# Optimization experiments

Measured on AMD Instinct MI355X. Metric: run time of the kernel, lower is better.

## Reference

```python
import jax, jax.numpy as jnp
import numpy as np

H = 8          # query heads
KVH = 1        # key/value heads
HD = 256       # head dim
ROPE_BASE = 10000.0


def _rotate_half(x):
    x1, x2 = x[..., : HD // 2], x[..., HD // 2 :]
    return jnp.concatenate((-x2, x1), axis=-1)


def _rope_cos_sin(position_ids):
    # position_ids: [B, S] int -> cos/sin: [B, S, HD]
    inv_freq = 1.0 / (ROPE_BASE ** (jnp.arange(0, HD, 2, dtype=jnp.float32) / HD))
    freqs = position_ids.astype(jnp.float32)[..., None] * inv_freq  # [B,S,HD/2]
    emb = jnp.concatenate((freqs, freqs), axis=-1)                  # [B,S,HD]
    return jnp.cos(emb), jnp.sin(emb)


def setup_inputs() -> dict:
    key = jax.random.key(0)
    ks = jax.random.split(key, 5)
    B, S, D = 2, 2048, 2048
    return {
        "hidden_states": jax.random.normal(ks[0], (B, S, D), dtype=jnp.float32),
        "attention_mask": jnp.zeros((B, 1, S, S), dtype=jnp.float32),
        "position_ids": jnp.broadcast_to(jnp.arange(S, dtype=jnp.int32), (B, S)),
        "Wq": jax.random.normal(ks[1], (D, H * HD), dtype=jnp.float32) * 0.02,
        "Wk": jax.random.normal(ks[2], (D, KVH * HD), dtype=jnp.float32) * 0.02,
        "Wv": jax.random.normal(ks[3], (D, KVH * HD), dtype=jnp.float32) * 0.02,
        "Wo": jax.random.normal(ks[4], (H * HD, D), dtype=jnp.float32) * 0.02,
    }


def reference(hidden_states, attention_mask, position_ids, Wq, Wk, Wv, Wo):
    B, S, D = hidden_states.shape
    # projections -> [B, heads, S, HD]
    q = jnp.einsum("bsd,df->bsf", hidden_states, Wq).reshape(B, S, H, HD).transpose(0, 2, 1, 3)
    k = jnp.einsum("bsd,df->bsf", hidden_states, Wk).reshape(B, S, KVH, HD).transpose(0, 2, 1, 3)
    v = jnp.einsum("bsd,df->bsf", hidden_states, Wv).reshape(B, S, KVH, HD).transpose(0, 2, 1, 3)

    cos, sin = _rope_cos_sin(position_ids)
    cos, sin = cos[:, None], sin[:, None]  # unsqueeze head dim
    q = q * cos + _rotate_half(q) * sin
    k = k * cos + _rotate_half(k) * sin

    # GQA: repeat kv heads to match query heads
    rep = H // KVH
    k = jnp.repeat(k, rep, axis=1)
    v = jnp.repeat(v, rep, axis=1)

    d_k = D // H  # matches torch code's scaling (== HD here)
    scores = jnp.einsum("bhqd,bhkd->bhqk", q, k) / jnp.sqrt(jnp.float32(d_k))
    scores = scores + attention_mask
    attn = jax.nn.softmax(scores, axis=-1)  # dropout p=0 / eval mode

    out = jnp.einsum("bhqk,bhkd->bhqd", attn, v)  # [B,H,S,HD]
    out = out.transpose(0, 2, 1, 3).reshape(B, S, H * HD)
    out = jnp.einsum("bsf,fd->bsd", out, Wo)
    return out
```

## Files before the change

kernel.cpp:

```cpp
#include <hip/hip_runtime.h>
#include <cmath>


typedef __bf16 bf16;
typedef __attribute__((ext_vector_type(8))) __bf16 bf16x8;
typedef __attribute__((ext_vector_type(4))) __bf16 bf16x4;
typedef __attribute__((ext_vector_type(4))) float f32x4;

#define S_LEN 2048
#define D_MODEL 2048
#define H_NUM 8
#define HDIM 256
#define KP 264
#define VP2 72

__device__ __forceinline__ void gl_lds16(const bf16* g, bf16* l) {
  __builtin_amdgcn_global_load_lds(
      (const __attribute__((address_space(1))) void*)g,
      (__attribute__((address_space(3))) void*)l, 16, 0, 0);
}

__global__ void cvt_bf16(const float* __restrict__ src, bf16* __restrict__ dst) {
  const int i = (blockIdx.x * 256 + threadIdx.x) * 4;
  const float4 v = *(const float4*)(src + i);
  bf16x4 o;
  o[0] = (bf16)v.x; o[1] = (bf16)v.y; o[2] = (bf16)v.z; o[3] = (bf16)v.w;
  *(bf16x4*)(dst + i) = o;
}

__global__ void tpose_cvt(const float* __restrict__ W, bf16* __restrict__ Wt,
                          int Ncols, int no0) {
  __shared__ float t[32][33];
  const int tx = threadIdx.x, ty = threadIdx.y;
  const int n0 = blockIdx.x * 32, k0 = blockIdx.y * 32;
#pragma unroll
  for (int i = 0; i < 4; ++i)
    t[ty + 8 * i][tx] = W[(size_t)(k0 + ty + 8 * i) * Ncols + (n0 + tx)];
  __syncthreads();
#pragma unroll
  for (int i = 0; i < 4; ++i)
    Wt[(size_t)(no0 + n0 + ty + 8 * i) * D_MODEL + (k0 + tx)] = (bf16)t[tx][ty + 8 * i];
}

__global__ __launch_bounds__(256)
void gemm_bf16(const bf16* __restrict__ A, const bf16* __restrict__ Wt,
               bf16* __restrict__ Cq, bf16* __restrict__ Ck, bf16* __restrict__ Cv,
               float* __restrict__ Cf, int M, int N, int mode) {
  __shared__ bf16 As[128 * 32];
  __shared__ bf16 Bs[128 * 32];
  const int tid = threadIdx.x;
  const int lane = tid & 63;
  const int wbase = tid & 192;
  const int c16 = lane & 15;
  const int quad = lane >> 4;
  const int wave = tid >> 6;
  const int wr = wave >> 1, wc = wave & 1;
  const int m0 = blockIdx.y * 128, n0 = blockIdx.x * 128;

  f32x4 acc[4][4];
#pragma unroll
  for (int i = 0; i < 4; ++i)
#pragma unroll
    for (int j = 0; j < 4; ++j)
#pragma unroll
      for (int r = 0; r < 4; ++r) acc[i][j][r] = 0.f;

  for (int k0 = 0; k0 < D_MODEL; k0 += 32) {
#pragma unroll
    for (int j = 0; j < 2; ++j) {
      const int bslot = j * 256 + wbase;
      const int slot = bslot + lane;
      const int row = slot >> 2, ch = slot & 3;
      gl_lds16(&A[(size_t)(m0 + row) * D_MODEL + k0 + ch * 8], &As[bslot * 8]);
      gl_lds16(&Wt[(size_t)(n0 + row) * D_MODEL + k0 + ch * 8], &Bs[bslot * 8]);
    }
    __syncthreads();
    bf16x8 af[4], bfr[4];
#pragma unroll
    for (int i = 0; i < 4; ++i)
      af[i] = *(const bf16x8*)&As[(wr * 64 + i * 16 + c16) * 32 + quad * 8];
#pragma unroll
    for (int j = 0; j < 4; ++j)
      bfr[j] = *(const bf16x8*)&Bs[(wc * 64 + j * 16 + c16) * 32 + quad * 8];
#pragma unroll
    for (int i = 0; i < 4; ++i)
#pragma unroll
      for (int j = 0; j < 4; ++j)
        acc[i][j] = __builtin_amdgcn_mfma_f32_16x16x32_bf16(af[i], bfr[j], acc[i][j], 0, 0, 0);
    __syncthreads();
  }

#pragma unroll
  for (int i = 0; i < 4; ++i)
#pragma unroll
    for (int j = 0; j < 4; ++j) {
      const int n = n0 + wc * 64 + j * 16 + c16;
#pragma unroll
      for (int r = 0; r < 4; ++r) {
        const int m = m0 + wr * 64 + i * 16 + quad * 4 + r;
        const float val = acc[i][j][r];
        if (mode == 1) {
          const int b = m >> 11, s = m & 2047;
          if (n0 < 2048) {
            const int h = n >> 8, hd = n & 255;
            Cq[((((size_t)b * H_NUM + h) * S_LEN + s) << 8) + hd] = (bf16)val;
          } else if (n0 < 2304) {
            Ck[((size_t)m << 8) + (n - 2048)] = (bf16)val;
          } else {
            Cv[((size_t)((b << 8) + (n - 2304)) << 11) + s] = (bf16)val;
          }
        } else {
          Cf[(size_t)m * D_MODEL + n] = val;
        }
      }
    }
}

#define ROPE_C (-0.07195578415606394f)

__global__ void rope_q_bf16(bf16* __restrict__ q, const int* __restrict__ pos) {
  const int idx = blockIdx.x * 256 + threadIdx.x;
  const int j = idx & 127;
  const int t = idx >> 7;
  const int s = t & 2047;
  const int bh = t >> 11;
  const int b = bh >> 3;
  const float p = (float)pos[(b << 11) + s];
  float sn, cs;
  sincosf(p * expf((float)j * ROPE_C), &sn, &cs);
  bf16* base = q + (((size_t)bh << 11) + s) * HDIM;
  const float x1 = (float)base[j], x2 = (float)base[j + 128];
  base[j] = (bf16)(x1 * cs - x2 * sn);
  base[j + 128] = (bf16)(x2 * cs + x1 * sn);
}

__global__ void rope_k_bf16(bf16* __restrict__ k, const int* __restrict__ pos) {
  const int idx = blockIdx.x * 256 + threadIdx.x;
  const int j = idx & 127;
  const int t = idx >> 7;
  const int s = t & 2047;
  const int b = t >> 11;
  const float p = (float)pos[(b << 11) + s];
  float sn, cs;
  sincosf(p * expf((float)j * ROPE_C), &sn, &cs);
  bf16* base = k + (size_t)t * HDIM;
  const float x1 = (float)base[j], x2 = (float)base[j + 128];
  base[j] = (bf16)(x1 * cs - x2 * sn);
  base[j + 128] = (bf16)(x2 * cs + x1 * sn);
}

__global__ __launch_bounds__(256, 2)
void flash_bf16(const bf16* __restrict__ qg, const bf16* __restrict__ kg,
                const bf16* __restrict__ vg, const float* __restrict__ msk,
                bf16* __restrict__ ao) {
  __shared__ bf16 Ks[64 * KP];
  __shared__ bf16 Vs[256 * VP2];
  __shared__ bf16 Ps[64 * VP2];

  const int tid = threadIdx.x;
  const int lane = tid & 63;
  const int w = tid >> 6;
  const int c16 = lane & 15;
  const int quad = lane >> 4;

  const int qbi = blockIdx.x & 31;
  const int h = (blockIdx.x >> 5) & 7;
  const int b = blockIdx.x >> 8;
  const int q0 = qbi * 64;

  const bf16* qbase = qg + ((((size_t)b * H_NUM + h) * S_LEN + q0) << 8);
  const bf16* kbase = kg + ((size_t)b << 19);
  const bf16* vbase = vg + ((size_t)b << 19);
  const float* mbase = msk + (size_t)b * S_LEN * S_LEN +
                       (size_t)(q0 + w * 16 + quad * 4) * S_LEN;

  bf16x8 qf[8];
#pragma unroll
  for (int kd = 0; kd < 8; ++kd)
    qf[kd] = *(const bf16x8*)&qbase[((w * 16 + c16) << 8) + kd * 32 + quad * 8];

  f32x4 oacc[16];
#pragma unroll
  for (int t = 0; t < 16; ++t)
#pragma unroll
    for (int r = 0; r < 4; ++r) oacc[t][r] = 0.f;
  float mrow[4] = {-1e30f, -1e30f, -1e30f, -1e30f};
  float lrow[4] = {0.f, 0.f, 0.f, 0.f};

  for (int k0 = 0; k0 < S_LEN; k0 += 64) {
    float ml[4][4];
#pragma unroll
    for (int ct = 0; ct < 4; ++ct)
#pragma unroll
      for (int r = 0; r < 4; ++r)
        ml[ct][r] = mbase[(size_t)r * S_LEN + k0 + ct * 16 + c16];

    __syncthreads();
#pragma unroll
    for (int i = 0; i < 8; ++i) {
      const int c = tid + i * 256;
      const int krow = c >> 5, kc = c & 31;
      *(bf16x8*)&Ks[krow * KP + kc * 8] =
          *(const bf16x8*)&kbase[((size_t)(k0 + krow) << 8) + kc * 8];
      const int vrow = c >> 3, vc = c & 7;
      *(bf16x8*)&Vs[vrow * VP2 + vc * 8] =
          *(const bf16x8*)&vbase[((size_t)vrow << 11) + k0 + vc * 8];
    }
    __syncthreads();

    f32x4 sc[4];
#pragma unroll
    for (int ct = 0; ct < 4; ++ct)
#pragma unroll
      for (int r = 0; r < 4; ++r) sc[ct][r] = 0.f;
#pragma unroll
    for (int kd = 0; kd < 8; ++kd) {
#pragma unroll
      for (int ct = 0; ct < 4; ++ct) {
        const bf16x8 bK = *(const bf16x8*)&Ks[(ct * 16 + c16) * KP + kd * 32 + quad * 8];
        sc[ct] = __builtin_amdgcn_mfma_f32_16x16x32_bf16(qf[kd], bK, sc[ct], 0, 0, 0);
      }
    }

    float sv[4][4];
#pragma unroll
    for (int ct = 0; ct < 4; ++ct)
#pragma unroll
      for (int r = 0; r < 4; ++r)
        sv[ct][r] = sc[ct][r] * 0.0625f + ml[ct][r];

    float mloc[4], al[4], pv[4][4], rs[4];
#pragma unroll
    for (int r = 0; r < 4; ++r)
      mloc[r] = fmaxf(fmaxf(sv[0][r], sv[1][r]), fmaxf(sv[2][r], sv[3][r]));
#pragma unroll
    for (int d = 1; d < 16; d <<= 1)
#pragma unroll
      for (int r = 0; r < 4; ++r) mloc[r] = fmaxf(mloc[r], __shfl_xor(mloc[r], d, 64));
#pragma unroll
    for (int r = 0; r < 4; ++r) {
      const float mn = fmaxf(mrow[r], mloc[r]);
      al[r] = __expf(mrow[r] - mn);
#pragma unroll
      for (int ct = 0; ct < 4; ++ct) pv[ct][r] = __expf(sv[ct][r] - mn);
      rs[r] = (pv[0][r] + pv[1][r]) + (pv[2][r] + pv[3][r]);
      mrow[r] = mn;
    }
#pragma unroll
    for (int d = 1; d < 16; d <<= 1)
#pragma unroll
      for (int r = 0; r < 4; ++r) rs[r] += __shfl_xor(rs[r], d, 64);
#pragma unroll
    for (int r = 0; r < 4; ++r) lrow[r] = lrow[r] * al[r] + rs[r];

#pragma unroll
    for (int ct = 0; ct < 4; ++ct)
#pragma unroll
      for (int r = 0; r < 4; ++r)
        Ps[(w * 16 + quad * 4 + r) * VP2 + ct * 16 + c16] = (bf16)pv[ct][r];
    __syncthreads();

    const bool need = (al[0] < 1.f) | (al[1] < 1.f) | (al[2] < 1.f) | (al[3] < 1.f);
    if (__ballot(need) != 0ull) {
#pragma unroll
      for (int t = 0; t < 16; ++t)
#pragma unroll
        for (int r = 0; r < 4; ++r) oacc[t][r] *= al[r];
    }

    const bf16x8 pa0 = *(const bf16x8*)&Ps[(w * 16 + c16) * VP2 + quad * 8];
    const bf16x8 pa1 = *(const bf16x8*)&Ps[(w * 16 + c16) * VP2 + 32 + quad * 8];
#pragma unroll
    for (int t = 0; t < 16; ++t) {
      const bf16x8 v0 = *(const bf16x8*)&Vs[(t * 16 + c16) * VP2 + quad * 8];
      const bf16x8 v1 = *(const bf16x8*)&Vs[(t * 16 + c16) * VP2 + 32 + quad * 8];
      oacc[t] = __builtin_amdgcn_mfma_f32_16x16x32_bf16(pa0, v0, oacc[t], 0, 0, 0);
      oacc[t] = __builtin_amdgcn_mfma_f32_16x16x32_bf16(pa1, v1, oacc[t], 0, 0, 0);
    }
  }

  float li[4];
#pragma unroll
  for (int r = 0; r < 4; ++r) li[r] = 1.f / lrow[r];
  bf16* obase = ao + (size_t)(b * S_LEN + q0 + w * 16 + quad * 4) * D_MODEL + (h << 8);
#pragma unroll
  for (int t = 0; t < 16; ++t)
#pragma unroll
    for (int r = 0; r < 4; ++r)
      obase[(size_t)r * D_MODEL + t * 16 + c16] = (bf16)(oacc[t][r] * li[r]);
}

extern "C" void kernel_launch(void* const* d_in, const int* in_sizes, int n_in,
                              void* d_out, int out_size, void* d_ws, size_t ws_size,
                              hipStream_t stream) {
  const float* hs   = (const float*)d_in[0];
  const float* mask = (const float*)d_in[1];
  const int*   pos  = (const int*)d_in[2];
  const float* Wq   = (const float*)d_in[3];
  const float* Wk   = (const float*)d_in[4];
  const float* Wv   = (const float*)d_in[5];
  const float* Wo   = (const float*)d_in[6];
  float* out = (float*)d_out;

  const int B = in_sizes[2] / S_LEN;
  const int M = B * S_LEN;

  char* wsc = (char*)d_ws;
  bf16* hsb = (bf16*)wsc;
  bf16* aob = hsb;
  size_t off = (size_t)M * D_MODEL * 2;
  bf16* Wqkvt = (bf16*)(wsc + off); off += (size_t)2560 * D_MODEL * 2;
  bf16* Wot   = (bf16*)(wsc + off); off += (size_t)D_MODEL * D_MODEL * 2;
  bf16* kb    = (bf16*)(wsc + off);
  bf16* vb    = kb + (size_t)M * HDIM;

  bf16* qb = (bf16*)d_out;

  const dim3 blk(256);
  const dim3 tb(32, 8);
  cvt_bf16<<<(M * D_MODEL) / 1024, blk, 0, stream>>>(hs, hsb);
  tpose_cvt<<<dim3(64, 64), tb, 0, stream>>>(Wq, Wqkvt, D_MODEL, 0);
  tpose_cvt<<<dim3(8, 64), tb, 0, stream>>>(Wk, Wqkvt, HDIM, 2048);
  tpose_cvt<<<dim3(8, 64), tb, 0, stream>>>(Wv, Wqkvt, HDIM, 2304);
  tpose_cvt<<<dim3(64, 64), tb, 0, stream>>>(Wo, Wot, D_MODEL, 0);

  gemm_bf16<<<dim3(20, M / 128), blk, 0, stream>>>(hsb, Wqkvt, qb, kb, vb, nullptr, M, 2560, 1);

  rope_q_bf16<<<(B * H_NUM * S_LEN * 128) / 256, blk, 0, stream>>>(qb, pos);
  rope_k_bf16<<<(B * S_LEN * 128) / 256, blk, 0, stream>>>(kb, pos);

  flash_bf16<<<B * H_NUM * (S_LEN / 64), blk, 0, stream>>>(qb, kb, vb, mask, aob);

  gemm_bf16<<<dim3(16, M / 128), blk, 0, stream>>>(aob, Wot, nullptr, nullptr, nullptr, out, M, D_MODEL, 3);
}
```

Baseline: 453.0 us.

## Double query rows per flash block and merge RoPE kernels into one launch

The flash attention block now handles 128 query rows instead of 64, with each wave processing two 16-row groups. Every K/V tile staged in shared memory is therefore reused for twice as many queries, which halves global K/V traffic and the number of block-level syncs per query. In exchange the kernel needs far more registers (two accumulator sets of 16 tiles each), its launch bounds drop to one block per SIMD slot, and the grid shrinks to 256 blocks. The Q and K RoPE kernels are also fused into a single launch to save one kernel launch.

```diff
diff --git a/kernel.cpp b/kernel.cpp
--- a/kernel.cpp
+++ b/kernel.cpp
@@ -118,44 +118,41 @@
 
 #define ROPE_C (-0.07195578415606394f)
 
-__global__ void rope_q_bf16(bf16* __restrict__ q, const int* __restrict__ pos) {
+__global__ void rope_all(bf16* __restrict__ q, bf16* __restrict__ k,
+                         const int* __restrict__ pos, int BHS) {
   const int idx = blockIdx.x * 256 + threadIdx.x;
   const int j = idx & 127;
   const int t = idx >> 7;
-  const int s = t & 2047;
-  const int bh = t >> 11;
-  const int b = bh >> 3;
-  const float p = (float)pos[(b << 11) + s];
   float sn, cs;
-  sincosf(p * expf((float)j * ROPE_C), &sn, &cs);
-  bf16* base = q + (((size_t)bh << 11) + s) * HDIM;
-  const float x1 = (float)base[j], x2 = (float)base[j + 128];
-  base[j] = (bf16)(x1 * cs - x2 * sn);
-  base[j + 128] = (bf16)(x2 * cs + x1 * sn);
-}
-
-__global__ void rope_k_bf16(bf16* __restrict__ k, const int* __restrict__ pos) {
-  const int idx = blockIdx.x * 256 + threadIdx.x;
-  const int j = idx & 127;
-  const int t = idx >> 7;
-  const int s = t & 2047;
-  const int b = t >> 11;
-  const float p = (float)pos[(b << 11) + s];
-  float sn, cs;
-  sincosf(p * expf((float)j * ROPE_C), &sn, &cs);
-  bf16* base = k + (size_t)t * HDIM;
-  const float x1 = (float)base[j], x2 = (float)base[j + 128];
-  base[j] = (bf16)(x1 * cs - x2 * sn);
-  base[j + 128] = (bf16)(x2 * cs + x1 * sn);
-}
-
-__global__ __launch_bounds__(256, 2)
+  if (t < BHS) {
+    const int s = t & 2047;
+    const int b = t >> 14;
+    const float p = (float)pos[(b << 11) + s];
+    sincosf(p * expf((float)j * ROPE_C), &sn, &cs);
+    bf16* base = q + ((size_t)t << 8);
+    const float x1 = (float)base[j], x2 = (float)base[j + 128];
+    base[j] = (bf16)(x1 * cs - x2 * sn);
+    base[j + 128] = (bf16)(x2 * cs + x1 * sn);
+  } else {
+    const int t2 = t - BHS;
+    const int s = t2 & 2047;
+    const int b = t2 >> 11;
+    const float p = (float)pos[(b << 11) + s];
+    sincosf(p * expf((float)j * ROPE_C), &sn, &cs);
+    bf16* base = k + ((size_t)t2 << 8);
+    const float x1 = (float)base[j], x2 = (float)base[j + 128];
+    base[j] = (bf16)(x1 * cs - x2 * sn);
+    base[j + 128] = (bf16)(x2 * cs + x1 * sn);
+  }
+}
+
+__global__ __launch_bounds__(256, 1)
 void flash_bf16(const bf16* __restrict__ qg, const bf16* __restrict__ kg,
                 const bf16* __restrict__ vg, const float* __restrict__ msk,
                 bf16* __restrict__ ao) {
   __shared__ bf16 Ks[64 * KP];
   __shared__ bf16 Vs[256 * VP2];
-  __shared__ bf16 Ps[64 * VP2];
+  __shared__ bf16 Ps[128 * VP2];
 
   const int tid = threadIdx.x;
   const int lane = tid & 63;
@@ -163,37 +160,47 @@
   const int c16 = lane & 15;
   const int quad = lane >> 4;
 
-  const int qbi = blockIdx.x & 31;
-  const int h = (blockIdx.x >> 5) & 7;
-  const int b = blockIdx.x >> 8;
-  const int q0 = qbi * 64;
+  const int qbi = blockIdx.x & 15;
+  const int h = (blockIdx.x >> 4) & 7;
+  const int b = blockIdx.x >> 7;
+  const int q0 = qbi * 128;
+  const int wrow = w * 32;
 
   const bf16* qbase = qg + ((((size_t)b * H_NUM + h) * S_LEN + q0) << 8);
   const bf16* kbase = kg + ((size_t)b << 19);
   const bf16* vbase = vg + ((size_t)b << 19);
   const float* mbase = msk + (size_t)b * S_LEN * S_LEN +
-                       (size_t)(q0 + w * 16 + quad * 4) * S_LEN;
-
-  bf16x8 qf[8];
-#pragma unroll
-  for (int kd = 0; kd < 8; ++kd)
-    qf[kd] = *(const bf16x8*)&qbase[((w * 16 + c16) << 8) + kd * 32 + quad * 8];
-
-  f32x4 oacc[16];
-#pragma unroll
-  for (int t = 0; t < 16; ++t)
-#pragma unroll
-    for (int r = 0; r < 4; ++r) oacc[t][r] = 0.f;
-  float mrow[4] = {-1e30f, -1e30f, -1e30f, -1e30f};
-  float lrow[4] = {0.f, 0.f, 0.f, 0.f};
+                       (size_t)(q0 + wrow + quad * 4) * S_LEN;
+
+  bf16x8 qf[2][8];
+#pragma unroll
+  for (int g = 0; g < 2; ++g)
+#pragma unroll
+    for (int kd = 0; kd < 8; ++kd)
+      qf[g][kd] = *(const bf16x8*)&qbase[((wrow + g * 16 + c16) << 8) + kd * 32 + quad * 8];
+
+  f32x4 oacc[2][16];
+#pragma unroll
+  for (int g = 0; g < 2; ++g)
+#pragma unroll
+    for (int t = 0; t < 16; ++t)
+#pragma unroll
+      for (int r = 0; r < 4; ++r) oacc[g][t][r] = 0.f;
+  float mrow[2][4], lrow[2][4];
+#pragma unroll
+  for (int g = 0; g < 2; ++g)
+#pragma unroll
+    for (int r = 0; r < 4; ++r) { mrow[g][r] = -1e30f; lrow[g][r] = 0.f; }
 
   for (int k0 = 0; k0 < S_LEN; k0 += 64) {
-    float ml[4][4];
-#pragma unroll
-    for (int ct = 0; ct < 4; ++ct)
-#pragma unroll
-      for (int r = 0; r < 4; ++r)
-        ml[ct][r] = mbase[(size_t)r * S_LEN + k0 + ct * 16 + c16];
+    float ml[2][4][4];
+#pragma unroll
+    for (int g = 0; g < 2; ++g)
+#pragma unroll
+      for (int ct = 0; ct < 4; ++ct)
+#pragma unroll
+        for (int r = 0; r < 4; ++r)
+          ml[g][ct][r] = mbase[(size_t)(g * 16 + r) * S_LEN + k0 + ct * 16 + c16];
 
     __syncthreads();
 #pragma unroll
@@ -208,86 +215,103 @@
     }
     __syncthreads();
 
-    f32x4 sc[4];
-#pragma unroll
-    for (int ct = 0; ct < 4; ++ct)
-#pragma unroll
-      for (int r = 0; r < 4; ++r) sc[ct][r] = 0.f;
+    f32x4 sc[2][4];
+#pragma unroll
+    for (int g = 0; g < 2; ++g)
+#pragma unroll
+      for (int ct = 0; ct < 4; ++ct)
+#pragma unroll
+        for (int r = 0; r < 4; ++r) sc[g][ct][r] = 0.f;
 #pragma unroll
     for (int kd = 0; kd < 8; ++kd) {
 #pragma unroll
       for (int ct = 0; ct < 4; ++ct) {
         const bf16x8 bK = *(const bf16x8*)&Ks[(ct * 16 + c16) * KP + kd * 32 + quad * 8];
-        sc[ct] = __builtin_amdgcn_mfma_f32_16x16x32_bf16(qf[kd], bK, sc[ct], 0, 0, 0);
+        sc[0][ct] = __builtin_amdgcn_mfma_f32_16x16x32_bf16(qf[0][kd], bK, sc[0][ct], 0, 0, 0);
+        sc[1][ct] = __builtin_amdgcn_mfma_f32_16x16x32_bf16(qf[1][kd], bK, sc[1][ct], 0, 0, 0);
       }
     }
 
-    float sv[4][4];
-#pragma unroll
-    for (int ct = 0; ct < 4; ++ct)
+    float al[2][4], pv[2][4][4];
+#pragma unroll
+    for (int g = 0; g < 2; ++g) {
+      float sv[4][4], mloc[4], rs[4];
+#pragma unroll
+      for (int ct = 0; ct < 4; ++ct)
+#pragma unroll
+        for (int r = 0; r < 4; ++r)
+          sv[ct][r] = sc[g][ct][r] * 0.0625f + ml[g][ct][r];
 #pragma unroll
       for (int r = 0; r < 4; ++r)
-        sv[ct][r] = sc[ct][r] * 0.0625f + ml[ct][r];
-
-    float mloc[4], al[4], pv[4][4], rs[4];
-#pragma unroll
-    for (int r = 0; r < 4; ++r)
-      mloc[r] = fmaxf(fmaxf(sv[0][r], sv[1][r]), fmaxf(sv[2][r], sv[3][r]));
-#pragma unroll
-    for (int d = 1; d < 16; d <<= 1)
-#pragma unroll
-      for (int r = 0; r < 4; ++r) mloc[r] = fmaxf(mloc[r], __shfl_xor(mloc[r], d, 64));
-#pragma unroll
-    for (int r = 0; r < 4; ++r) {
-      const float mn = fmaxf(mrow[r], mloc[r]);
-      al[r] = __expf(mrow[r] - mn);
-#pragma unroll
-      for (int ct = 0; ct < 4; ++ct) pv[ct][r] = __expf(sv[ct][r] - mn);
-      rs[r] = (pv[0][r] + pv[1][r]) + (pv[2][r] + pv[3][r]);
-      mrow[r] = mn;
-    }
-#pragma unroll
-    for (int d = 1; d < 16; d <<= 1)
-#pragma unroll
-      for (int r = 0; r < 4; ++r) rs[r] += __shfl_xor(rs[r], d, 64);
-#pragma unroll
-    for (int r = 0; r < 4; ++r) lrow[r] = lrow[r] * al[r] + rs[r];
-
-#pragma unroll
-    for (int ct = 0; ct < 4; ++ct)
-#pragma unroll
-      for (int r = 0; r < 4; ++r)
-        Ps[(w * 16 + quad * 4 + r) * VP2 + ct * 16 + c16] = (bf16)pv[ct][r];
-    __syncthreads();
-
-    const bool need = (al[0] < 1.f) | (al[1] < 1.f) | (al[2] < 1.f) | (al[3] < 1.f);
+        mloc[r] = fmaxf(fmaxf(sv[0][r], sv[1][r]), fmaxf(sv[2][r], sv[3][r]));
+#pragma unroll
+      for (int d = 1; d < 16; d <<= 1)
+#pragma unroll
+        for (int r = 0; r < 4; ++r) mloc[r] = fmaxf(mloc[r], __shfl_xor(mloc[r], d, 64));
+#pragma unroll
+      for (int r = 0; r < 4; ++r) {
+        const float mn = fmaxf(mrow[g][r], mloc[r]);
+        al[g][r] = __expf(mrow[g][r] - mn);
+#pragma unroll
+        for (int ct = 0; ct < 4; ++ct) pv[g][ct][r] = __expf(sv[ct][r] - mn);
+        rs[r] = (pv[g][0][r] + pv[g][1][r]) + (pv[g][2][r] + pv[g][3][r]);
+        mrow[g][r] = mn;
+      }
+#pragma unroll
+      for (int d = 1; d < 16; d <<= 1)
+#pragma unroll
+        for (int r = 0; r < 4; ++r) rs[r] += __shfl_xor(rs[r], d, 64);
+#pragma unroll
+      for (int r = 0; r < 4; ++r) lrow[g][r] = lrow[g][r] * al[g][r] + rs[r];
+    }
+
+#pragma unroll
+    for (int g = 0; g < 2; ++g)
+#pragma unroll
+      for (int ct = 0; ct < 4; ++ct)
+#pragma unroll
+        for (int r = 0; r < 4; ++r)
+          Ps[(wrow + g * 16 + quad * 4 + r) * VP2 + ct * 16 + c16] = (bf16)pv[g][ct][r];
+    __syncthreads();
+
+    const bool need = (al[0][0] < 1.f) | (al[0][1] < 1.f) | (al[0][2] < 1.f) | (al[0][3] < 1.f) |
+                      (al[1][0] < 1.f) | (al[1][1] < 1.f) | (al[1][2] < 1.f) | (al[1][3] < 1.f);
     if (__ballot(need) != 0ull) {
 #pragma unroll
-      for (int t = 0; t < 16; ++t)
-#pragma unroll
-        for (int r = 0; r < 4; ++r) oacc[t][r] *= al[r];
-    }
-
-    const bf16x8 pa0 = *(const bf16x8*)&Ps[(w * 16 + c16) * VP2 + quad * 8];
-    const bf16x8 pa1 = *(const bf16x8*)&Ps[(w * 16 + c16) * VP2 + 32 + quad * 8];
+      for (int g = 0; g < 2; ++g)
+#pragma unroll
+        for (int t = 0; t < 16; ++t)
+#pragma unroll
+          for (int r = 0; r < 4; ++r) oacc[g][t][r] *= al[g][r];
+    }
+
+    const bf16x8 pa00 = *(const bf16x8*)&Ps[(wrow + c16) * VP2 + quad * 8];
+    const bf16x8 pa01 = *(const bf16x8*)&Ps[(wrow + c16) * VP2 + 32 + quad * 8];
+    const bf16x8 pa10 = *(const bf16x8*)&Ps[(wrow + 16 + c16) * VP2 + quad * 8];
+    const bf16x8 pa11 = *(const bf16x8*)&Ps[(wrow + 16 + c16) * VP2 + 32 + quad * 8];
 #pragma unroll
     for (int t = 0; t < 16; ++t) {
       const bf16x8 v0 = *(const bf16x8*)&Vs[(t * 16 + c16) * VP2 + quad * 8];
       const bf16x8 v1 = *(const bf16x8*)&Vs[(t * 16 + c16) * VP2 + 32 + quad * 8];
-      oacc[t] = __builtin_amdgcn_mfma_f32_16x16x32_bf16(pa0, v0, oacc[t], 0, 0, 0);
-      oacc[t] = __builtin_amdgcn_mfma_f32_16x16x32_bf16(pa1, v1, oacc[t], 0, 0, 0);
+      oacc[0][t] = __builtin_amdgcn_mfma_f32_16x16x32_bf16(pa00, v0, oacc[0][t], 0, 0, 0);
+      oacc[0][t] = __builtin_amdgcn_mfma_f32_16x16x32_bf16(pa01, v1, oacc[0][t], 0, 0, 0);
+      oacc[1][t] = __builtin_amdgcn_mfma_f32_16x16x32_bf16(pa10, v0, oacc[1][t], 0, 0, 0);
+      oacc[1][t] = __builtin_amdgcn_mfma_f32_16x16x32_bf16(pa11, v1, oacc[1][t], 0, 0, 0);
     }
   }
 
-  float li[4];
-#pragma unroll
-  for (int r = 0; r < 4; ++r) li[r] = 1.f / lrow[r];
-  bf16* obase = ao + (size_t)(b * S_LEN + q0 + w * 16 + quad * 4) * D_MODEL + (h << 8);
-#pragma unroll
-  for (int t = 0; t < 16; ++t)
-#pragma unroll
-    for (int r = 0; r < 4; ++r)
-      obase[(size_t)r * D_MODEL + t * 16 + c16] = (bf16)(oacc[t][r] * li[r]);
+#pragma unroll
+  for (int g = 0; g < 2; ++g) {
+    float li[4];
+#pragma unroll
+    for (int r = 0; r < 4; ++r) li[r] = 1.f / lrow[g][r];
+    bf16* obase = ao + (size_t)(b * S_LEN + q0 + wrow + g * 16 + quad * 4) * D_MODEL + (h << 8);
+#pragma unroll
+    for (int t = 0; t < 16; ++t)
+#pragma unroll
+      for (int r = 0; r < 4; ++r)
+        obase[(size_t)r * D_MODEL + t * 16 + c16] = (bf16)(oacc[g][t][r] * li[r]);
+  }
 }
 
 extern "C" void kernel_launch(void* const* d_in, const int* in_sizes, int n_in,
@@ -326,10 +350,10 @@
 
   gemm_bf16<<<dim3(20, M / 128), blk, 0, stream>>>(hsb, Wqkvt, qb, kb, vb, nullptr, M, 2560, 1);
 
-  rope_q_bf16<<<(B * H_NUM * S_LEN * 128) / 256, blk, 0, stream>>>(qb, pos);
-  rope_k_bf16<<<(B * S_LEN * 128) / 256, blk, 0, stream>>>(kb, pos);
-
-  flash_bf16<<<B * H_NUM * (S_LEN / 64), blk, 0, stream>>>(qb, kb, vb, mask, aob);
+  rope_all<<<(B * (H_NUM + 1) * S_LEN * 128) / 256, blk, 0, stream>>>(
+      qb, kb, pos, B * H_NUM * S_LEN);
+
+  flash_bf16<<<B * H_NUM * (S_LEN / 128), blk, 0, stream>>>(qb, kb, vb, mask, aob);
 
   gemm_bf16<<<dim3(16, M / 128), blk, 0, stream>>>(aob, Wot, nullptr, nullptr, nullptr, out, M, D_MODEL, 3);
 }
```

New measurement: 477.1 us. +5.3%, slower.
